# Kernel tuning notes

Hardware: AMD Instinct MI355X
Metric: run time of the kernel (lower is better)

## Reference

```python
import jax, jax.numpy as jnp
import numpy as np

N_NODES = 50000
N_EDGES = 800000
IN_DIM = 128
HIDDEN = 64
HEADS = 4
EPS = 1e-5
NEG_SLOPE = 0.2  # PyG GATConv default


def setup_inputs() -> dict:
    key = jax.random.key(0)
    ks = jax.random.split(key, 12)
    s = 0.1
    x = jax.random.normal(ks[0], (N_NODES, IN_DIM), jnp.float32)
    edge_index = jax.random.randint(ks[1], (2, N_EDGES), 0, N_NODES, dtype=jnp.int64)
    return {
        "x": x,
        "edge_index": edge_index,
        # BatchNorm1d(input_dim)
        "gamma1": jnp.ones((IN_DIM,), jnp.float32),
        "beta1": jnp.zeros((IN_DIM,), jnp.float32),
        # GATConv(IN_DIM, HIDDEN, heads=HEADS, concat=True)
        "W1": jax.random.normal(ks[2], (IN_DIM, HEADS * HIDDEN), jnp.float32) * s,
        "att_src1": jax.random.normal(ks[3], (HEADS, HIDDEN), jnp.float32) * s,
        "att_dst1": jax.random.normal(ks[4], (HEADS, HIDDEN), jnp.float32) * s,
        "bias1": jnp.zeros((HEADS * HIDDEN,), jnp.float32),
        # BatchNorm1d(hidden*heads)
        "gamma2": jnp.ones((HEADS * HIDDEN,), jnp.float32),
        "beta2": jnp.zeros((HEADS * HIDDEN,), jnp.float32),
        # GATConv(hidden*heads, HIDDEN, heads=HEADS, concat=False)
        "W2": jax.random.normal(ks[5], (HEADS * HIDDEN, HEADS * HIDDEN), jnp.float32) * s,
        "att_src2": jax.random.normal(ks[6], (HEADS, HIDDEN), jnp.float32) * s,
        "att_dst2": jax.random.normal(ks[7], (HEADS, HIDDEN), jnp.float32) * s,
        "bias2": jnp.zeros((HIDDEN,), jnp.float32),
    }


def batchnorm(x, gamma, beta):
    # training-mode BatchNorm1d: biased variance over the batch dim
    m = x.mean(axis=0)
    v = x.var(axis=0)
    return (x - m) * jax.lax.rsqrt(v + EPS) * gamma + beta


def gat_conv(h, src, dst, W, att_src, att_dst, bias, concat):
    n = h.shape[0]
    hl = (h @ W).reshape(n, HEADS, -1)                 # [N, H, C]
    a_src = (hl * att_src).sum(-1)                     # [N, H]
    a_dst = (hl * att_dst).sum(-1)                     # [N, H]
    e = jax.nn.leaky_relu(a_src[src] + a_dst[dst], NEG_SLOPE)  # [E, H]
    # segment softmax over destination neighborhoods
    e_max = jax.ops.segment_max(e, dst, num_segments=n)
    e = jnp.exp(e - e_max[dst])
    denom = jax.ops.segment_sum(e, dst, num_segments=n)
    alpha = e / denom[dst]                             # [E, H]
    msg = alpha[:, :, None] * hl[src]                  # [E, H, C]
    out = jax.ops.segment_sum(msg, dst, num_segments=n)  # [N, H, C]
    out = out.reshape(n, -1) if concat else out.mean(axis=1)
    return out + bias


def reference(x, edge_index, gamma1, beta1, W1, att_src1, att_dst1, bias1,
              gamma2, beta2, W2, att_src2, att_dst2, bias2):
    n = x.shape[0]
    loop = jnp.arange(n, dtype=edge_index.dtype)
    src = jnp.concatenate([edge_index[0], loop])  # add_self_loops=True
    dst = jnp.concatenate([edge_index[1], loop])
    h = batchnorm(x, gamma1, beta1)
    h = gat_conv(h, src, dst, W1, att_src1, att_dst1, bias1, concat=True)
    h = batchnorm(h, gamma2, beta2)
    h = jax.nn.relu(h)
    h = gat_conv(h, src, dst, W2, att_src2, att_dst2, bias2, concat=False)
    return h
```

## Files before the change

### kernel.cpp

```cpp
#include <hip/hip_runtime.h>

#define N_NODES 50000
#define N_EDGES 800000
#define E_TOT   (N_EDGES + N_NODES)
#define F1      128
#define F2      256
#define EPS     1e-5f
#define SLOPE   0.2f
#define DCAP    96

typedef __bf16 bf16x8 __attribute__((ext_vector_type(8)));
typedef float  f32x4  __attribute__((ext_vector_type(4)));

__device__ __forceinline__ float bf2f(unsigned short b) {
    return __uint_as_float((unsigned)b << 16);
}
__device__ __forceinline__ unsigned short f2bf(float f) {
    unsigned u = __float_as_uint(f);
    u += 0x7fffu + ((u >> 16) & 1u);
    return (unsigned short)(u >> 16);
}

__global__ __launch_bounds__(256)
void bn_stats_f32(const float* __restrict__ X,
                  float* __restrict__ sums, float* __restrict__ sumsq) {
    int t = threadIdx.x;
    int cgi = t & 31, rl = t >> 5;
    float4 s = {0.f, 0.f, 0.f, 0.f}, q = {0.f, 0.f, 0.f, 0.f};
    for (int r = blockIdx.x * 8 + rl; r < N_NODES; r += gridDim.x * 8) {
        float4 v = ((const float4*)(X + (size_t)r * F1))[cgi];
        s.x += v.x; s.y += v.y; s.z += v.z; s.w += v.w;
        q.x += v.x * v.x; q.y += v.y * v.y; q.z += v.z * v.z; q.w += v.w * v.w;
    }
    __shared__ float4 ls[256], lq[256];
    ls[t] = s; lq[t] = q;
    __syncthreads();
    if (t < 32) {
        float4 S = ls[t], Q = lq[t];
        for (int j = 1; j < 8; j++) {
            float4 a = ls[j * 32 + t], b = lq[j * 32 + t];
            S.x += a.x; S.y += a.y; S.z += a.z; S.w += a.w;
            Q.x += b.x; Q.y += b.y; Q.z += b.z; Q.w += b.w;
        }
        atomicAdd(&sums[t * 4 + 0], S.x); atomicAdd(&sums[t * 4 + 1], S.y);
        atomicAdd(&sums[t * 4 + 2], S.z); atomicAdd(&sums[t * 4 + 3], S.w);
        atomicAdd(&sumsq[t * 4 + 0], Q.x); atomicAdd(&sumsq[t * 4 + 1], Q.y);
        atomicAdd(&sumsq[t * 4 + 2], Q.z); atomicAdd(&sumsq[t * 4 + 3], Q.w);
    }
}

__global__ __launch_bounds__(256)
void bn_stats_bf16(const unsigned short* __restrict__ X,
                   float* __restrict__ sums, float* __restrict__ sumsq) {
    int t = threadIdx.x;
    int cgi = t & 31, rl = t >> 5;
    float s[8], q[8];
#pragma unroll
    for (int j = 0; j < 8; j++) { s[j] = 0.f; q[j] = 0.f; }
    for (int r = blockIdx.x * 8 + rl; r < N_NODES; r += gridDim.x * 8) {
        uint4 raw = ((const uint4*)(X + (size_t)r * F2))[cgi];
        float v[8];
        v[0] = bf2f(raw.x & 0xffff); v[1] = bf2f(raw.x >> 16);
        v[2] = bf2f(raw.y & 0xffff); v[3] = bf2f(raw.y >> 16);
        v[4] = bf2f(raw.z & 0xffff); v[5] = bf2f(raw.z >> 16);
        v[6] = bf2f(raw.w & 0xffff); v[7] = bf2f(raw.w >> 16);
#pragma unroll
        for (int j = 0; j < 8; j++) { s[j] += v[j]; q[j] += v[j] * v[j]; }
    }
    __shared__ float ls[256 * 8], lq[256 * 8];
#pragma unroll
    for (int j = 0; j < 8; j++) { ls[t * 8 + j] = s[j]; lq[t * 8 + j] = q[j]; }
    __syncthreads();
    if (t < 32) {
        float S[8], Q[8];
#pragma unroll
        for (int j = 0; j < 8; j++) { S[j] = ls[t * 8 + j]; Q[j] = lq[t * 8 + j]; }
        for (int rr = 1; rr < 8; rr++)
#pragma unroll
            for (int j = 0; j < 8; j++) {
                S[j] += ls[(rr * 32 + t) * 8 + j];
                Q[j] += lq[(rr * 32 + t) * 8 + j];
            }
#pragma unroll
        for (int j = 0; j < 8; j++) {
            atomicAdd(&sums[t * 8 + j], S[j]);
            atomicAdd(&sumsq[t * 8 + j], Q[j]);
        }
    }
}

__global__ void bn_coef(const float* __restrict__ sums, const float* __restrict__ sumsq,
                        const float* __restrict__ gamma, const float* __restrict__ beta,
                        float* __restrict__ scale, float* __restrict__ shift, int K) {
    int t = blockIdx.x * 64 + threadIdx.x;
    if (t < K) {
        const float invN = 1.f / (float)N_NODES;
        float m  = sums[t] * invN;
        float vv = sumsq[t] * invN - m * m;
        float sc = rsqrtf(vv + EPS) * gamma[t];
        scale[t] = sc;
        shift[t] = fmaf(-m, sc, beta[t]);
    }
}

__global__ void fill_direct(const int* __restrict__ esrc, const int* __restrict__ edst,
                            int* __restrict__ deg, int* __restrict__ col) {
    int i = blockIdx.x * 256 + threadIdx.x;
    if (i < N_EDGES) {
        int d = edst[i];
        int slot = atomicAdd(&deg[d], 1);
        if (slot < DCAP) col[d * DCAP + slot] = esrc[i];
    } else if (i < E_TOT) {
        int n = i - N_EDGES;
        int slot = atomicAdd(&deg[n], 1);
        if (slot < DCAP) col[n * DCAP + slot] = n;
    }
}

__device__ __forceinline__ void prep_frag(const float* __restrict__ W, __bf16* __restrict__ Wf,
                                          int tid) {
    int lane = tid & 63;
    int nt = (tid >> 6) & 15;
    int ks = tid >> 10;
    int q = lane >> 4, c = lane & 15;
#pragma unroll
    for (int j = 0; j < 8; j++)
        Wf[(size_t)tid * 8 + j] = (__bf16)W[(size_t)(ks * 32 + q * 8 + j) * F2 + nt * 16 + c];
}
__global__ void prep_w_all(const float* __restrict__ W1, const float* __restrict__ W2,
                           __bf16* __restrict__ Wf1, __bf16* __restrict__ Wf2) {
    int tid = blockIdx.x * 256 + threadIdx.x;
    const int n1 = (F1 / 32) * 16 * 64;
    const int n2 = (F2 / 32) * 16 * 64;
    if (tid < n1) prep_frag(W1, Wf1, tid);
    else if (tid < n1 + n2) prep_frag(W2, Wf2, tid - n1);
}

template<int K, bool RELU, bool ABF16>
__global__ __launch_bounds__(64)
void gemm_mfma(const void* __restrict__ Xv,
               const float* __restrict__ scale, const float* __restrict__ shift,
               const __bf16* __restrict__ Wf,
               const float* __restrict__ att_s, const float* __restrict__ att_d,
               __bf16* __restrict__ hlb, float* __restrict__ a_src, float* __restrict__ a_dst) {
    int lane = threadIdx.x;
    int q = lane >> 4, c = lane & 15;
    int mrow = blockIdx.x * 32;
    int row0 = mrow + c, row1 = mrow + 16 + c;
    int r0 = row0 < N_NODES ? row0 : N_NODES - 1;
    int r1 = row1 < N_NODES ? row1 : N_NODES - 1;

    f32x4 acc[2][16];
#pragma unroll
    for (int m = 0; m < 2; m++)
#pragma unroll
        for (int nt = 0; nt < 16; nt++) acc[m][nt] = (f32x4){0.f, 0.f, 0.f, 0.f};

    for (int ks = 0; ks < K / 32; ks++) {
        int kb = ks * 32 + q * 8;
        float scv[8], sfv[8];
        *(float4*)scv       = *(const float4*)(scale + kb);
        *(float4*)(scv + 4) = *(const float4*)(scale + kb + 4);
        *(float4*)sfv       = *(const float4*)(shift + kb);
        *(float4*)(sfv + 4) = *(const float4*)(shift + kb + 4);
        bf16x8 afr[2];
#pragma unroll
        for (int m = 0; m < 2; m++) {
            int rr = m ? r1 : r0;
            float y[8];
            if (ABF16) {
                const unsigned short* xp = (const unsigned short*)Xv + (size_t)rr * K + kb;
                uint4 raw = *(const uint4*)xp;
                y[0] = bf2f(raw.x & 0xffff); y[1] = bf2f(raw.x >> 16);
                y[2] = bf2f(raw.y & 0xffff); y[3] = bf2f(raw.y >> 16);
                y[4] = bf2f(raw.z & 0xffff); y[5] = bf2f(raw.z >> 16);
                y[6] = bf2f(raw.w & 0xffff); y[7] = bf2f(raw.w >> 16);
            } else {
                const float* xp = (const float*)Xv + (size_t)rr * K + kb;
                *(float4*)y       = *(const float4*)xp;
                *(float4*)(y + 4) = *(const float4*)(xp + 4);
            }
            bf16x8 a;
#pragma unroll
            for (int j = 0; j < 8; j++) {
                float yy = fmaf(y[j], scv[j], sfv[j]);
                if (RELU) yy = fmaxf(yy, 0.f);
                a[j] = (__bf16)yy;
            }
            afr[m] = a;
        }
#pragma unroll
        for (int nt = 0; nt < 16; nt++) {
            bf16x8 b = *(const bf16x8*)(Wf + ((size_t)(ks * 16 + nt) * 64 + lane) * 8);
            acc[0][nt] = __builtin_amdgcn_mfma_f32_16x16x32_bf16(afr[0], b, acc[0][nt], 0, 0, 0);
            acc[1][nt] = __builtin_amdgcn_mfma_f32_16x16x32_bf16(afr[1], b, acc[1][nt], 0, 0, 0);
        }
    }

#pragma unroll
    for (int m = 0; m < 2; m++) {
        int rowb = mrow + m * 16 + q * 4;
#pragma unroll
        for (int r = 0; r < 4; r++) {
            int row = rowb + r;
            if (row < N_NODES) {
#pragma unroll
                for (int nt = 0; nt < 16; nt++)
                    hlb[(size_t)row * F2 + nt * 16 + c] = (__bf16)acc[m][nt][r];
            }
        }
    }
    float asv[16], adv[16];
#pragma unroll
    for (int nt = 0; nt < 16; nt++) { asv[nt] = att_s[nt * 16 + c]; adv[nt] = att_d[nt * 16 + c]; }
#pragma unroll
    for (int m = 0; m < 2; m++) {
#pragma unroll
        for (int r = 0; r < 4; r++) {
            int row = mrow + m * 16 + q * 4 + r;
            float ps0 = 0.f, ps1 = 0.f, ps2 = 0.f, ps3 = 0.f;
            float pd0 = 0.f, pd1 = 0.f, pd2 = 0.f, pd3 = 0.f;
#pragma unroll
            for (int j = 0; j < 4; j++) {
                ps0 = fmaf(acc[m][j][r],      asv[j],      ps0);
                ps1 = fmaf(acc[m][4 + j][r],  asv[4 + j],  ps1);
                ps2 = fmaf(acc[m][8 + j][r],  asv[8 + j],  ps2);
                ps3 = fmaf(acc[m][12 + j][r], asv[12 + j], ps3);
                pd0 = fmaf(acc[m][j][r],      adv[j],      pd0);
                pd1 = fmaf(acc[m][4 + j][r],  adv[4 + j],  pd1);
                pd2 = fmaf(acc[m][8 + j][r],  adv[8 + j],  pd2);
                pd3 = fmaf(acc[m][12 + j][r], adv[12 + j], pd3);
            }
#pragma unroll
            for (int off = 1; off < 16; off <<= 1) {
                ps0 += __shfl_xor(ps0, off); ps1 += __shfl_xor(ps1, off);
                ps2 += __shfl_xor(ps2, off); ps3 += __shfl_xor(ps3, off);
                pd0 += __shfl_xor(pd0, off); pd1 += __shfl_xor(pd1, off);
                pd2 += __shfl_xor(pd2, off); pd3 += __shfl_xor(pd3, off);
            }
            if (c == 0 && row < N_NODES) {
                float4 vs; vs.x = ps0; vs.y = ps1; vs.z = ps2; vs.w = ps3;
                float4 vd; vd.x = pd0; vd.y = pd1; vd.z = pd2; vd.w = pd3;
                *(float4*)(a_src + row * 4) = vs;
                *(float4*)(a_dst + row * 4) = vd;
            }
        }
    }
}

template<bool MEAN>
__global__ __launch_bounds__(128)
void node_aggr(const int* __restrict__ degp, const int* __restrict__ col,
               const float* __restrict__ a_src, const float* __restrict__ a_dst,
               const ushort2* __restrict__ hlb, const float* __restrict__ bias,
               void* __restrict__ outv) {
    int n = blockIdx.x, t = threadIdx.x;
    int deg = degp[n]; deg = deg < DCAP ? deg : DCAP;
    int start = n * DCAP;
    __shared__ float se[DCAP * 4];
    __shared__ int   scol[DCAP];
    __shared__ float wred[8];
    __shared__ float sdenom[4];
    int h4 = t & 3;
    float adn = a_dst[n * 4 + h4];
    float local = 0.f;
    if (t < deg) scol[t] = col[start + t];
    __syncthreads();
    for (int p = t; p < deg * 4; p += 128) {
        int i = p >> 2;
        float v = a_src[scol[i] * 4 + h4] + adn;
        v = v > 0.f ? v : SLOPE * v;
        float e = __expf(v);
        se[p] = e;
        local += e;
    }
#pragma unroll
    for (int off = 4; off < 64; off <<= 1) local += __shfl_xor(local, off);
    if ((t & 63) < 4) wred[(t >> 6) * 4 + h4] = local;
    __syncthreads();
    if (t < 4) sdenom[t] = wred[t] + wred[t + 4];
    __syncthreads();

    int h = t >> 5;
    float rd = 1.f / sdenom[h];
    float acc0 = 0.f, acc1 = 0.f;
#pragma unroll 8
    for (int i = 0; i < deg; i++) {
        float e = se[i * 4 + h];
        ushort2 hv = hlb[(size_t)scol[i] * (F2 / 2) + t];
        acc0 = fmaf(e, bf2f(hv.x), acc0);
        acc1 = fmaf(e, bf2f(hv.y), acc1);
    }
    acc0 *= rd; acc1 *= rd;
    if (MEAN) {
        __shared__ float sred[256];
        sred[2 * t] = acc0; sred[2 * t + 1] = acc1;
        __syncthreads();
        if (t < 64)
            ((float*)outv)[(size_t)n * 64 + t] =
                0.25f * (sred[t] + sred[t + 64] + sred[t + 128] + sred[t + 192]) + bias[t];
    } else {
        ushort2 ov; ov.x = f2bf(acc0); ov.y = f2bf(acc1);
        ((ushort2*)outv)[(size_t)n * (F2 / 2) + t] = ov;
    }
}

extern "C" void kernel_launch(void* const* d_in, const int* in_sizes, int n_in,
                              void* d_out, int out_size, void* d_ws, size_t ws_size,
                              hipStream_t stream) {
    const float* x        = (const float*)d_in[0];
    const int*   edge     = (const int*)  d_in[1];
    const float* gamma1   = (const float*)d_in[2];
    const float* beta1    = (const float*)d_in[3];
    const float* W1       = (const float*)d_in[4];
    const float* att_src1 = (const float*)d_in[5];
    const float* att_dst1 = (const float*)d_in[6];
    const float* gamma2   = (const float*)d_in[8];
    const float* beta2    = (const float*)d_in[9];
    const float* W2       = (const float*)d_in[10];
    const float* att_src2 = (const float*)d_in[11];
    const float* att_dst2 = (const float*)d_in[12];
    const float* bias2    = (const float*)d_in[13];
    float* out = (float*)d_out;

    const int* esrc = edge;
    const int* edst = edge + N_EDGES;

    float* wsf = (float*)d_ws;
    size_t o = 0;
    __bf16* hlb   = (__bf16*)(wsf + o); o += (size_t)N_NODES * F2 / 2;
    __bf16* acc1b = (__bf16*)(wsf + o); o += (size_t)N_NODES * F2 / 2;
    __bf16* Wf1 = (__bf16*)(wsf + o); o += (size_t)F1 * F2 / 2;
    __bf16* Wf2 = (__bf16*)(wsf + o); o += (size_t)F2 * F2 / 2;
    float* a_src1 = wsf + o; o += N_NODES * 4;
    float* a_dst1 = wsf + o; o += N_NODES * 4;
    float* a_src2 = wsf + o; o += N_NODES * 4;
    float* a_dst2 = wsf + o; o += N_NODES * 4;
    float* scale1 = wsf + o; o += F1;
    float* shift1 = wsf + o; o += F1;
    float* scale2 = wsf + o; o += F2;
    float* shift2 = wsf + o; o += F2;
    size_t zstart = o;
    float* sums1  = wsf + o; o += F1;
    float* sumsq1 = wsf + o; o += F1;
    float* sums2  = wsf + o; o += F2;
    float* sumsq2 = wsf + o; o += F2;
    int* deg    = (int*)(wsf + o); o += N_NODES;
    size_t zbytes = (o - zstart) * sizeof(float);
    int* col    = (int*)(wsf + o); o += (size_t)N_NODES * DCAP;

    hipMemsetAsync(wsf + zstart, 0, zbytes, stream);

    fill_direct<<<(E_TOT + 255) / 256, 256, 0, stream>>>(esrc, edst, deg, col);

    prep_w_all<<<48, 256, 0, stream>>>(W1, W2, Wf1, Wf2);

    const int gemm_grid = (N_NODES + 31) / 32;

    bn_stats_f32<<<256, 256, 0, stream>>>(x, sums1, sumsq1);
    bn_coef<<<(F1 + 63) / 64, 64, 0, stream>>>(sums1, sumsq1, gamma1, beta1, scale1, shift1, F1);
    gemm_mfma<F1, false, false><<<gemm_grid, 64, 0, stream>>>(x, scale1, shift1, Wf1,
                                                              att_src1, att_dst1,
                                                              hlb, a_src1, a_dst1);
    node_aggr<false><<<N_NODES, 128, 0, stream>>>(deg, col, a_src1, a_dst1,
                                                  (const ushort2*)hlb, nullptr, acc1b);

    bn_stats_bf16<<<256, 256, 0, stream>>>((const unsigned short*)acc1b, sums2, sumsq2);
    bn_coef<<<(F2 + 63) / 64, 64, 0, stream>>>(sums2, sumsq2, gamma2, beta2, scale2, shift2, F2);
    gemm_mfma<F2, true, true><<<gemm_grid, 64, 0, stream>>>(acc1b, scale2, shift2, Wf2,
                                                            att_src2, att_dst2,
                                                            hlb, a_src2, a_dst2);
    node_aggr<true><<<N_NODES, 128, 0, stream>>>(deg, col, a_src2, a_dst2,
                                                 (const ushort2*)hlb, bias2, out);
}
```

Before: 447.2 us.

## Fold attention projections into GEMM as extra column tile and permute hidden layout

Precomputes W·att_src and W·att_dst as a 17th MFMA column tile, so the attention logits come straight out of the GEMM accumulators instead of a per-row dot product with a shuffle reduction. The GEMM output is also written in a column-permuted layout, so each lane stores 16 contiguous bf16 values as two 128-bit stores instead of scattered 2-byte stores. The permutation is propagated into the BN2 coefficients, the second-layer weight rows and the mean reduction in node_aggr. This adds one more MFMA tile per k-step and computes the logits from a bf16-rounded folded weight, which may shift numerics slightly.

Result: faster. 427.2 us (-4.5%).

```diff
diff --git a/kernel.cpp b/kernel.cpp
--- a/kernel.cpp
+++ b/kernel.cpp
@@ -8,6 +8,8 @@
 #define EPS     1e-5f
 #define SLOPE   0.2f
 #define DCAP    96
+#define NT      17
+
 
 typedef __bf16 bf16x8 __attribute__((ext_vector_type(8)));
 typedef float  f32x4  __attribute__((ext_vector_type(4)));
@@ -89,17 +91,19 @@
     }
 }
 
+template<bool PERM>
 __global__ void bn_coef(const float* __restrict__ sums, const float* __restrict__ sumsq,
                         const float* __restrict__ gamma, const float* __restrict__ beta,
                         float* __restrict__ scale, float* __restrict__ shift, int K) {
     int t = blockIdx.x * 64 + threadIdx.x;
     if (t < K) {
+        int src = PERM ? ((t & 15) * 16 + (t >> 4)) : t;
         const float invN = 1.f / (float)N_NODES;
         float m  = sums[t] * invN;
         float vv = sumsq[t] * invN - m * m;
-        float sc = rsqrtf(vv + EPS) * gamma[t];
+        float sc = rsqrtf(vv + EPS) * gamma[src];
         scale[t] = sc;
-        shift[t] = fmaf(-m, sc, beta[t]);
+        shift[t] = fmaf(-m, sc, beta[src]);
     }
 }
 
@@ -117,23 +121,42 @@
     }
 }
 
-__device__ __forceinline__ void prep_frag(const float* __restrict__ W, __bf16* __restrict__ Wf,
-                                          int tid) {
+template<int K, bool PERM>
+__device__ __forceinline__ void prep_frag(const float* __restrict__ W,
+                                          const float* __restrict__ att_s,
+                                          const float* __restrict__ att_d,
+                                          __bf16* __restrict__ Wf, int tid) {
     int lane = tid & 63;
-    int nt = (tid >> 6) & 15;
-    int ks = tid >> 10;
+    int nt = (tid >> 6) % NT;
+    int ks = (tid >> 6) / NT;
     int q = lane >> 4, c = lane & 15;
 #pragma unroll
-    for (int j = 0; j < 8; j++)
-        Wf[(size_t)tid * 8 + j] = (__bf16)W[(size_t)(ks * 32 + q * 8 + j) * F2 + nt * 16 + c];
+    for (int j = 0; j < 8; j++) {
+        int k = ks * 32 + q * 8 + j;
+        int kt = PERM ? ((k & 15) * 16 + (k >> 4)) : k;
+        float v;
+        if (nt < 16) {
+            v = W[(size_t)kt * F2 + nt * 16 + c];
+        } else if (c < 8) {
+            const float* av = (c < 4) ? att_s : att_d;
+            int h = c & 3;
+            float sacc = 0.f;
+            for (int u = 0; u < 64; u++)
+                sacc = fmaf(W[(size_t)kt * F2 + h * 64 + u], av[h * 64 + u], sacc);
+            v = sacc;
+        } else v = 0.f;
+        Wf[(size_t)tid * 8 + j] = (__bf16)v;
+    }
 }
 __global__ void prep_w_all(const float* __restrict__ W1, const float* __restrict__ W2,
+                           const float* __restrict__ as1, const float* __restrict__ ad1,
+                           const float* __restrict__ as2, const float* __restrict__ ad2,
                            __bf16* __restrict__ Wf1, __bf16* __restrict__ Wf2) {
     int tid = blockIdx.x * 256 + threadIdx.x;
-    const int n1 = (F1 / 32) * 16 * 64;
-    const int n2 = (F2 / 32) * 16 * 64;
-    if (tid < n1) prep_frag(W1, Wf1, tid);
-    else if (tid < n1 + n2) prep_frag(W2, Wf2, tid - n1);
+    const int n1 = (F1 / 32) * NT * 64;
+    const int n2 = (F2 / 32) * NT * 64;
+    if (tid < n1) prep_frag<F1, false>(W1, as1, ad1, Wf1, tid);
+    else if (tid < n1 + n2) prep_frag<F2, true>(W2, as2, ad2, Wf2, tid - n1);
 }
 
 template<int K, bool RELU, bool ABF16>
@@ -141,7 +164,6 @@
 void gemm_mfma(const void* __restrict__ Xv,
                const float* __restrict__ scale, const float* __restrict__ shift,
                const __bf16* __restrict__ Wf,
-               const float* __restrict__ att_s, const float* __restrict__ att_d,
                __bf16* __restrict__ hlb, float* __restrict__ a_src, float* __restrict__ a_dst) {
     int lane = threadIdx.x;
     int q = lane >> 4, c = lane & 15;
@@ -150,11 +172,11 @@
     int r0 = row0 < N_NODES ? row0 : N_NODES - 1;
     int r1 = row1 < N_NODES ? row1 : N_NODES - 1;
 
-    f32x4 acc[2][16];
+    f32x4 acc[2][NT];
 #pragma unroll
     for (int m = 0; m < 2; m++)
 #pragma unroll
-        for (int nt = 0; nt < 16; nt++) acc[m][nt] = (f32x4){0.f, 0.f, 0.f, 0.f};
+        for (int nt = 0; nt < NT; nt++) acc[m][nt] = (f32x4){0.f, 0.f, 0.f, 0.f};
 
     for (int ks = 0; ks < K / 32; ks++) {
         int kb = ks * 32 + q * 8;
@@ -190,8 +212,8 @@
             afr[m] = a;
         }
 #pragma unroll
-        for (int nt = 0; nt < 16; nt++) {
-            bf16x8 b = *(const bf16x8*)(Wf + ((size_t)(ks * 16 + nt) * 64 + lane) * 8);
+        for (int nt = 0; nt < NT; nt++) {
+            bf16x8 b = *(const bf16x8*)(Wf + ((size_t)(ks * NT + nt) * 64 + lane) * 8);
             acc[0][nt] = __builtin_amdgcn_mfma_f32_16x16x32_bf16(afr[0], b, acc[0][nt], 0, 0, 0);
             acc[1][nt] = __builtin_amdgcn_mfma_f32_16x16x32_bf16(afr[1], b, acc[1][nt], 0, 0, 0);
         }
@@ -199,50 +221,21 @@
 
 #pragma unroll
     for (int m = 0; m < 2; m++) {
-        int rowb = mrow + m * 16 + q * 4;
-#pragma unroll
-        for (int r = 0; r < 4; r++) {
-            int row = rowb + r;
-            if (row < N_NODES) {
-#pragma unroll
-                for (int nt = 0; nt < 16; nt++)
-                    hlb[(size_t)row * F2 + nt * 16 + c] = (__bf16)acc[m][nt][r];
-            }
-        }
-    }
-    float asv[16], adv[16];
-#pragma unroll
-    for (int nt = 0; nt < 16; nt++) { asv[nt] = att_s[nt * 16 + c]; adv[nt] = att_d[nt * 16 + c]; }
-#pragma unroll
-    for (int m = 0; m < 2; m++) {
 #pragma unroll
         for (int r = 0; r < 4; r++) {
             int row = mrow + m * 16 + q * 4 + r;
-            float ps0 = 0.f, ps1 = 0.f, ps2 = 0.f, ps3 = 0.f;
-            float pd0 = 0.f, pd1 = 0.f, pd2 = 0.f, pd3 = 0.f;
-#pragma unroll
-            for (int j = 0; j < 4; j++) {
-                ps0 = fmaf(acc[m][j][r],      asv[j],      ps0);
-                ps1 = fmaf(acc[m][4 + j][r],  asv[4 + j],  ps1);
-                ps2 = fmaf(acc[m][8 + j][r],  asv[8 + j],  ps2);
-                ps3 = fmaf(acc[m][12 + j][r], asv[12 + j], ps3);
-                pd0 = fmaf(acc[m][j][r],      adv[j],      pd0);
-                pd1 = fmaf(acc[m][4 + j][r],  adv[4 + j],  pd1);
-                pd2 = fmaf(acc[m][8 + j][r],  adv[8 + j],  pd2);
-                pd3 = fmaf(acc[m][12 + j][r], adv[12 + j], pd3);
-            }
-#pragma unroll
-            for (int off = 1; off < 16; off <<= 1) {
-                ps0 += __shfl_xor(ps0, off); ps1 += __shfl_xor(ps1, off);
-                ps2 += __shfl_xor(ps2, off); ps3 += __shfl_xor(ps3, off);
-                pd0 += __shfl_xor(pd0, off); pd1 += __shfl_xor(pd1, off);
-                pd2 += __shfl_xor(pd2, off); pd3 += __shfl_xor(pd3, off);
-            }
-            if (c == 0 && row < N_NODES) {
-                float4 vs; vs.x = ps0; vs.y = ps1; vs.z = ps2; vs.w = ps3;
-                float4 vd; vd.x = pd0; vd.y = pd1; vd.z = pd2; vd.w = pd3;
-                *(float4*)(a_src + row * 4) = vs;
-                *(float4*)(a_dst + row * 4) = vd;
+            if (row < N_NODES) {
+                unsigned pk[8];
+#pragma unroll
+                for (int e = 0; e < 8; e++)
+                    pk[e] = (unsigned)f2bf(acc[m][2 * e][r]) |
+                            ((unsigned)f2bf(acc[m][2 * e + 1][r]) << 16);
+                uint4* dst = (uint4*)(hlb + (size_t)row * F2 + c * 16);
+                dst[0] = *(uint4*)pk;
+                dst[1] = *(uint4*)(pk + 4);
+                float av = acc[m][16][r];
+                if (c < 4)           a_src[row * 4 + c] = av;
+                else if (c < 8)      a_dst[row * 4 + (c - 4)] = av;
             }
         }
     }
@@ -281,7 +274,7 @@
     if (t < 4) sdenom[t] = wred[t] + wred[t + 4];
     __syncthreads();
 
-    int h = t >> 5;
+    int h = (t & 7) >> 1;
     float rd = 1.f / sdenom[h];
     float acc0 = 0.f, acc1 = 0.f;
 #pragma unroll 8
@@ -294,7 +287,9 @@
     acc0 *= rd; acc1 *= rd;
     if (MEAN) {
         __shared__ float sred[256];
-        sred[2 * t] = acc0; sred[2 * t + 1] = acc1;
+        int p0 = 2 * t;
+        int c0 = (p0 & 15) * 16 + (p0 >> 4);
+        sred[c0] = acc0; sred[c0 + 16] = acc1;
         __syncthreads();
         if (t < 64)
             ((float*)outv)[(size_t)n * 64 + t] =
@@ -330,8 +325,8 @@
     size_t o = 0;
     __bf16* hlb   = (__bf16*)(wsf + o); o += (size_t)N_NODES * F2 / 2;
     __bf16* acc1b = (__bf16*)(wsf + o); o += (size_t)N_NODES * F2 / 2;
-    __bf16* Wf1 = (__bf16*)(wsf + o); o += (size_t)F1 * F2 / 2;
-    __bf16* Wf2 = (__bf16*)(wsf + o); o += (size_t)F2 * F2 / 2;
+    __bf16* Wf1 = (__bf16*)(wsf + o); o += (size_t)(F1 / 32) * NT * 64 * 8 / 2;
+    __bf16* Wf2 = (__bf16*)(wsf + o); o += (size_t)(F2 / 32) * NT * 64 * 8 / 2;
     float* a_src1 = wsf + o; o += N_NODES * 4;
     float* a_dst1 = wsf + o; o += N_NODES * 4;
     float* a_src2 = wsf + o; o += N_NODES * 4;
@@ -353,22 +348,23 @@
 
     fill_direct<<<(E_TOT + 255) / 256, 256, 0, stream>>>(esrc, edst, deg, col);
 
-    prep_w_all<<<48, 256, 0, stream>>>(W1, W2, Wf1, Wf2);
+    prep_w_all<<<51, 256, 0, stream>>>(W1, W2, att_src1, att_dst1, att_src2, att_dst2,
+                                       Wf1, Wf2);
 
     const int gemm_grid = (N_NODES + 31) / 32;
 
     bn_stats_f32<<<256, 256, 0, stream>>>(x, sums1, sumsq1);
-    bn_coef<<<(F1 + 63) / 64, 64, 0, stream>>>(sums1, sumsq1, gamma1, beta1, scale1, shift1, F1);
+    bn_coef<false><<<(F1 + 63) / 64, 64, 0, stream>>>(sums1, sumsq1, gamma1, beta1,
+                                                      scale1, shift1, F1);
     gemm_mfma<F1, false, false><<<gemm_grid, 64, 0, stream>>>(x, scale1, shift1, Wf1,
-                                                              att_src1, att_dst1,
                                                               hlb, a_src1, a_dst1);
     node_aggr<false><<<N_NODES, 128, 0, stream>>>(deg, col, a_src1, a_dst1,
                                                   (const ushort2*)hlb, nullptr, acc1b);
 
     bn_stats_bf16<<<256, 256, 0, stream>>>((const unsigned short*)acc1b, sums2, sumsq2);
-    bn_coef<<<(F2 + 63) / 64, 64, 0, stream>>>(sums2, sumsq2, gamma2, beta2, scale2, shift2, F2);
+    bn_coef<true><<<(F2 + 63) / 64, 64, 0, stream>>>(sums2, sumsq2, gamma2, beta2,
+                                                     scale2, shift2, F2);
     gemm_mfma<F2, true, true><<<gemm_grid, 64, 0, stream>>>(acc1b, scale2, shift2, Wf2,
-                                                            att_src2, att_dst2,
                                                             hlb, a_src2, a_dst2);
     node_aggr<true><<<N_NODES, 128, 0, stream>>>(deg, col, a_src2, a_dst2,
                                                  (const ushort2*)hlb, bias2, out);
```
